# Optimization experiments

Hardware: AMD Instinct MI355X
Metric: run time of the kernel (lower is better)

## Reference

```python
import jax, jax.numpy as jnp
import numpy as np

K_H, K_W = 3, 3
STRIDE, PAD = 1, 1
GN_GROUPS = 32
EPS = 1e-5


def setup_inputs() -> dict:
    key = jax.random.key(0)
    k1, k2, k3 = jax.random.split(key, 3)
    B, C, H, W = 4, 256, 64, 64
    Cout = 256
    x = jax.random.normal(k1, (B, C, H, W), jnp.float32)
    offset = jax.random.normal(k2, (B, 2 * K_H * K_W, H, W), jnp.float32)
    weight = jax.random.normal(k3, (Cout, C, K_H, K_W), jnp.float32) * 0.02
    gamma = jnp.ones((Cout,), jnp.float32)
    beta = jnp.zeros((Cout,), jnp.float32)
    return {"x": x, "offset": offset, "weight": weight, "gamma": gamma, "beta": beta}


def _deform_conv(x, offset, weight):
    B, C, H, W = x.shape
    Cout = weight.shape[0]
    K = K_H * K_W
    Ho = (H + 2 * PAD - K_H) // STRIDE + 1
    Wo = (W + 2 * PAD - K_W) // STRIDE + 1
    ky, kx = jnp.meshgrid(jnp.arange(K_H), jnp.arange(K_W), indexing='ij')
    ky = ky.reshape(K).astype(x.dtype)
    kx = kx.reshape(K).astype(x.dtype)
    # base sampling positions per kernel tap
    py_base = (jnp.arange(Ho) * STRIDE - PAD).astype(x.dtype)[None, :] + ky[:, None]  # [K,Ho]
    px_base = (jnp.arange(Wo) * STRIDE - PAD).astype(x.dtype)[None, :] + kx[:, None]  # [K,Wo]
    off = offset.reshape(B, K, 2, Ho, Wo)  # mmcv layout: (dy, dx) pairs per tap
    py = py_base[None, :, :, None] + off[:, :, 0]  # [B,K,Ho,Wo]
    px = px_base[None, :, None, :] + off[:, :, 1]  # [B,K,Ho,Wo]
    y0 = jnp.floor(py)
    x0 = jnp.floor(px)
    ly = py - y0
    lx = px - x0
    xf = x.reshape(B, C, H * W)

    def gather(yi, xi):
        valid = (yi >= 0) & (yi <= H - 1) & (xi >= 0) & (xi <= W - 1)
        yc = jnp.clip(yi, 0, H - 1).astype(jnp.int32)
        xc = jnp.clip(xi, 0, W - 1).astype(jnp.int32)
        idx = yc * W + xc  # [B,K,Ho,Wo]
        vals = jax.vmap(lambda xb, ib: xb[:, ib])(xf, idx)  # [B,C,K,Ho,Wo]
        return vals * valid[:, None].astype(x.dtype)

    g00 = gather(y0, x0)
    g01 = gather(y0, x0 + 1)
    g10 = gather(y0 + 1, x0)
    g11 = gather(y0 + 1, x0 + 1)
    wy = ly[:, None]  # [B,1,K,Ho,Wo]
    wx = lx[:, None]
    val = ((1 - wy) * (1 - wx) * g00 + (1 - wy) * wx * g01
           + wy * (1 - wx) * g10 + wy * wx * g11)  # [B,C,K,Ho,Wo]
    return jnp.einsum('bckhw,ock->bohw', val, weight.reshape(Cout, C, K))


def reference(x, offset, weight, gamma, beta):
    y = _deform_conv(x, offset, weight)  # [B,Cout,Ho,Wo]
    B, C, H, W = y.shape
    yg = y.reshape(B, GN_GROUPS, C // GN_GROUPS, H, W)
    mean = jnp.mean(yg, axis=(2, 3, 4), keepdims=True)
    var = jnp.var(yg, axis=(2, 3, 4), keepdims=True)
    yn = ((yg - mean) * jax.lax.rsqrt(var + EPS)).reshape(B, C, H, W)
    out = yn * gamma[None, :, None, None] + beta[None, :, None, None]
    return jax.nn.relu(out)
```

## Files before the change

### kernel.cpp

```cpp
#include <hip/hip_runtime.h>

typedef unsigned short ushort_t;
typedef __bf16 bf16x8 __attribute__((ext_vector_type(8)));
typedef float f32x4 __attribute__((ext_vector_type(4)));
typedef void __attribute__((address_space(1))) gvoid_t;
typedef void __attribute__((address_space(3))) lvoid_t;

__device__ __forceinline__ float bflo(unsigned u) { return __builtin_bit_cast(float, u << 16); }
__device__ __forceinline__ float bfhi(unsigned u) { return __builtin_bit_cast(float, u & 0xffff0000u); }
__device__ __forceinline__ float bf2f(ushort_t v) {
  return __builtin_bit_cast(float, ((unsigned)v) << 16);
}
__device__ __forceinline__ unsigned f2bf_bits(float f) {
  unsigned u = __builtin_bit_cast(unsigned, f);
  return (u + 0x7fffu + ((u >> 16) & 1u)) >> 16;
}
__device__ __forceinline__ ushort_t f2bf(float f) { return (ushort_t)f2bf_bits(f); }

__global__ __launch_bounds__(256) void k_prep_w(const float* __restrict__ w,
                                                ushort_t* __restrict__ wb) {
  const int idx = blockIdx.x * 256 + threadIdx.x;
  const float* src = w + (size_t)idx * 9;
  #pragma unroll
  for (int k = 0; k < 9; ++k)
    wb[(k << 16) + idx] = f2bf(src[k]);
}

__global__ __launch_bounds__(256) void k_prep_x(const float* __restrict__ x,
                                                ushort_t* __restrict__ xt) {
  __shared__ ushort_t tile[64][68];
  const int bid = blockIdx.x;
  const int b = bid >> 8;
  const int ct = (bid >> 6) & 3;
  const int pt = bid & 63;
  const int t = threadIdx.x;
  const float* xb = x + ((size_t)(b * 256 + ct * 64)) * 4096 + pt * 64;
  #pragma unroll
  for (int i = 0; i < 16; ++i) {
    const int idx = t + 256 * i;
    const int c_l = idx >> 6, p_l = idx & 63;
    tile[c_l][p_l] = f2bf(xb[(size_t)c_l * 4096 + p_l]);
  }
  __syncthreads();
  ushort_t* xo = xt + ((size_t)(b * 4096 + pt * 64)) * 256 + ct * 64;
  #pragma unroll
  for (int i = 0; i < 16; ++i) {
    const int idx = t + 256 * i;
    const int p_l = idx >> 6, c_l = idx & 63;
    xo[(size_t)p_l * 256 + c_l] = tile[c_l][p_l];
  }
}

struct SMeta {
  float w00, w01, w10, w11;
  int i00, i01, i10, i11;
};
__device__ __forceinline__ SMeta meta_for(int h, int gw, int k, float oy, float ox) {
  SMeta m;
  const float py = (float)(h - 1 + k / 3) + oy;
  const float px = (float)(gw - 1 + k % 3) + ox;
  const float fy = floorf(py), fx = floorf(px);
  const float ly = py - fy, lx = px - fx;
  const int iy0 = (int)fy, ix0 = (int)fx;
  const float vy0 = (iy0 >= 0 && iy0 < 64) ? 1.f : 0.f;
  const float vy1 = (iy0 >= -1 && iy0 < 63) ? 1.f : 0.f;
  const float vx0 = (ix0 >= 0 && ix0 < 64) ? 1.f : 0.f;
  const float vx1 = (ix0 >= -1 && ix0 < 63) ? 1.f : 0.f;
  m.w00 = (1.f - ly) * (1.f - lx) * vy0 * vx0;
  m.w01 = (1.f - ly) * lx * vy0 * vx1;
  m.w10 = ly * (1.f - lx) * vy1 * vx0;
  m.w11 = ly * lx * vy1 * vx1;
  const int cy0 = min(max(iy0, 0), 63), cy1 = min(max(iy0 + 1, 0), 63);
  const int cx0 = min(max(ix0, 0), 63), cx1 = min(max(ix0 + 1, 0), 63);
  m.i00 = (cy0 * 64 + cx0) * 256;
  m.i01 = (cy0 * 64 + cx1) * 256;
  m.i10 = (cy1 * 64 + cx0) * 256;
  m.i11 = (cy1 * 64 + cx1) * 256;
  return m;
}

__device__ __forceinline__ unsigned lerp_pack(unsigned a, unsigned b, unsigned c, unsigned d,
                                              float w00, float w01, float w10, float w11) {
  float lo = w00 * bflo(a) + w01 * bflo(b) + w10 * bflo(c) + w11 * bflo(d);
  float hi = w00 * bfhi(a) + w01 * bfhi(b) + w10 * bfhi(c) + w11 * bfhi(d);
  return f2bf_bits(lo) | (f2bf_bits(hi) << 16);
}

template <int KH>
__device__ __forceinline__ void run_gemm(const float* __restrict__ offb,
                                         const ushort_t* __restrict__ xtb,
                                         const ushort_t* __restrict__ wb,
                                         ushort_t* Ab, ushort_t* Bb,
                                         int h, int s_w, int c8, int t,
                                         int wm, int wn, int wq, int wr,
                                         f32x4 (&acc)[2][4]) {
  float oy[5], ox[5];
  #pragma unroll
  for (int i = 0; i < 5; ++i) {
    oy[i] = offb[(2 * (KH * 4 + i)) * 4096];
    ox[i] = offb[(2 * (KH * 4 + i) + 1) * 4096];
  }

#define GATHER(N)                                                \
  {                                                              \
    const int c_ = KH * 18 + (N);                                \
    const int tap_ = c_ >> 2;                                    \
    const int loc_ = tap_ - KH * 4;                              \
    const int c0_ = (c_ & 3) << 6;                               \
    m = meta_for(h, s_w, tap_, oy[loc_], ox[loc_]);              \
    const int cc_ = c0_ + c8 * 8;                                \
    q00 = *(const uint4*)(xtb + m.i00 + cc_);                    \
    q01 = *(const uint4*)(xtb + m.i01 + cc_);                    \
    q10 = *(const uint4*)(xtb + m.i10 + cc_);                    \
    q11 = *(const uint4*)(xtb + m.i11 + cc_);                    \
  }

#define B_ISSUE(N, BUF)                                                                        \
  {                                                                                            \
    const int c_ = KH * 18 + (N);                                                              \
    const int tap_ = c_ >> 2;                                                                  \
    const int c0_ = (c_ & 3) << 6;                                                             \
    _Pragma("unroll") for (int i_ = 0; i_ < 4; ++i_) {                                         \
      const int idx_ = i_ * 512 + t;                                                           \
      const int row_ = idx_ >> 3, slot_ = idx_ & 7;                                            \
      const ushort_t* g_ = wb + (tap_ << 16) + row_ * 256 + c0_ + ((slot_ ^ (row_ & 7)) << 3); \
      __builtin_amdgcn_global_load_lds(                                                        \
          (gvoid_t*)g_, (lvoid_t*)((char*)Bb + (BUF) * 32768 + idx_ * 16), 16, 0, 0);          \
    }                                                                                          \
  }

#define A_WRITE(BUF)                                                         \
  {                                                                          \
    uint4 r;                                                                 \
    r.x = lerp_pack(q00.x, q01.x, q10.x, q11.x, m.w00, m.w01, m.w10, m.w11); \
    r.y = lerp_pack(q00.y, q01.y, q10.y, q11.y, m.w00, m.w01, m.w10, m.w11); \
    r.z = lerp_pack(q00.z, q01.z, q10.z, q11.z, m.w00, m.w01, m.w10, m.w11); \
    r.w = lerp_pack(q00.w, q01.w, q10.w, q11.w, m.w00, m.w01, m.w10, m.w11); \
    *(uint4*)&Ab[(BUF) * 4096 + s_w * 64 + ((c8 ^ (s_w & 7)) << 3)] = r;     \
  }

  {
    SMeta m;
    uint4 q00, q01, q10, q11;
    B_ISSUE(0, 0);
    GATHER(0);
    A_WRITE(0);
  }
  __syncthreads();

  #pragma unroll
  for (int n = 0; n < 18; ++n) {
    const int cur = n & 1;
    const int nb = cur ^ 1;
    SMeta m;
    uint4 q00, q01, q10, q11;
    if (n < 17) {
      B_ISSUE(n + 1, nb);
      GATHER(n + 1);
    }
    #pragma unroll
    for (int ks = 0; ks < 2; ++ks) {
      bf16x8 af[2], bfr[4];
      #pragma unroll
      for (int tm = 0; tm < 2; ++tm) {
        const int row = wm * 32 + tm * 16 + wr;
        const int slot = (ks * 4 + wq) ^ (row & 7);
        af[tm] = *(const bf16x8*)&Ab[cur * 4096 + row * 64 + slot * 8];
      }
      #pragma unroll
      for (int tn = 0; tn < 4; ++tn) {
        const int row = wn * 64 + tn * 16 + wr;
        const int slot = (ks * 4 + wq) ^ (row & 7);
        bfr[tn] = *(const bf16x8*)&Bb[cur * 16384 + row * 64 + slot * 8];
      }
      #pragma unroll
      for (int tm = 0; tm < 2; ++tm)
        #pragma unroll
        for (int tn = 0; tn < 4; ++tn)
          acc[tm][tn] =
              __builtin_amdgcn_mfma_f32_16x16x32_bf16(af[tm], bfr[tn], acc[tm][tn], 0, 0, 0);
    }
    if (n < 17) {
      A_WRITE(nb);
      __syncthreads();
    }
  }
#undef GATHER
#undef B_ISSUE
#undef A_WRITE
}

__global__ __launch_bounds__(512) void k_gemm(const float* __restrict__ off,
                                              const ushort_t* __restrict__ xt,
                                              const ushort_t* __restrict__ wb,
                                              ushort_t* __restrict__ y0,
                                              ushort_t* __restrict__ y1) {
  __shared__ __attribute__((aligned(16))) ushort_t Abuf[2][64 * 64];
  __shared__ __attribute__((aligned(16))) ushort_t Bbuf[2][256 * 64];

  const int bid = blockIdx.x;
  const int rowid = bid & 255;
  const int kh = bid >> 8;
  const int lb = ((rowid & 7) << 5) | (rowid >> 3);
  const int b = lb >> 6;
  const int h = lb & 63;
  const int t = threadIdx.x;
  const int wave = t >> 6;
  const int lane = t & 63;
  const int wq = lane >> 4;
  const int wr = lane & 15;
  const int wm = wave >> 2;
  const int wn = wave & 3;
  const int s_w = t >> 3;
  const int c8 = t & 7;

  const f32x4 zero = {0.f, 0.f, 0.f, 0.f};
  f32x4 acc[2][4];
  #pragma unroll
  for (int i = 0; i < 2; ++i)
    #pragma unroll
    for (int j = 0; j < 4; ++j) acc[i][j] = zero;

  const ushort_t* xtb = xt + (size_t)b * 4096 * 256;
  const float* offb = off + (size_t)b * 18 * 4096 + h * 64 + s_w;

  if (kh == 0)
    run_gemm<0>(offb, xtb, wb, &Abuf[0][0], &Bbuf[0][0], h, s_w, c8, t, wm, wn, wq, wr, acc);
  else
    run_gemm<1>(offb, xtb, wb, &Abuf[0][0], &Bbuf[0][0], h, s_w, c8, t, wm, wn, wq, wr, acc);

  ushort_t* yb = (kh ? y1 : y0) + ((size_t)(b * 4096 + h * 64)) * 256;
  #pragma unroll
  for (int tm = 0; tm < 2; ++tm) {
    #pragma unroll
    for (int tn = 0; tn < 4; ++tn) {
      const int o = wn * 64 + tn * 16 + wr;
      #pragma unroll
      for (int r2 = 0; r2 < 4; ++r2) {
        const int ww = wm * 32 + tm * 16 + wq * 4 + r2;
        yb[ww * 256 + o] = f2bf(acc[tm][tn][r2]);
      }
    }
  }
}

__global__ __launch_bounds__(256) void k_comb(const ushort_t* __restrict__ y0,
                                              const ushort_t* __restrict__ y1,
                                              ushort_t* __restrict__ yc,
                                              float* __restrict__ stats) {
  const int bid = blockIdx.x;
  const int lb = ((bid & 7) << 5) | (bid >> 3);
  const int b = lb >> 6;
  const int sc = lb & 63;
  const int t = threadIdx.x;
  const int og = t & 31;
  const int s0 = t >> 5;
  const size_t base = ((size_t)(b * 4096 + sc * 64)) * 256 + og * 8;
  float sum = 0.f, ss = 0.f;
  #pragma unroll
  for (int i = 0; i < 8; ++i) {
    const size_t o8 = base + (size_t)(s0 + i * 8) * 256;
    const uint4 a = *(const uint4*)(y0 + o8);
    const uint4 c = *(const uint4*)(y1 + o8);
    uint4 r;
    {
      float vl = bflo(a.x) + bflo(c.x), vh = bfhi(a.x) + bfhi(c.x);
      r.x = f2bf_bits(vl) | (f2bf_bits(vh) << 16);
      sum += vl + vh; ss += vl * vl + vh * vh;
    }
    {
      float vl = bflo(a.y) + bflo(c.y), vh = bfhi(a.y) + bfhi(c.y);
      r.y = f2bf_bits(vl) | (f2bf_bits(vh) << 16);
      sum += vl + vh; ss += vl * vl + vh * vh;
    }
    {
      float vl = bflo(a.z) + bflo(c.z), vh = bfhi(a.z) + bfhi(c.z);
      r.z = f2bf_bits(vl) | (f2bf_bits(vh) << 16);
      sum += vl + vh; ss += vl * vl + vh * vh;
    }
    {
      float vl = bflo(a.w) + bflo(c.w), vh = bfhi(a.w) + bfhi(c.w);
      r.w = f2bf_bits(vl) | (f2bf_bits(vh) << 16);
      sum += vl + vh; ss += vl * vl + vh * vh;
    }
    *(uint4*)(yc + o8) = r;
  }
  sum += __shfl_xor(sum, 32, 64);
  ss += __shfl_xor(ss, 32, 64);
  if ((t & 63) < 32) {
    atomicAdd(&stats[(b * 32 + og) * 2], sum);
    atomicAdd(&stats[(b * 32 + og) * 2 + 1], ss);
  }
}

__global__ __launch_bounds__(256) void k_apply(const ushort_t* __restrict__ yc,
                                               const float* __restrict__ stats,
                                               const float* __restrict__ gamma,
                                               const float* __restrict__ beta,
                                               float* __restrict__ out) {
  __shared__ float tile[64][65];
  __shared__ float sm[8], sr[8], sg[64], sb[64];
  const int bid = blockIdx.x;
  const int lb = ((bid & 7) << 7) | (bid >> 3);
  const int b = lb >> 8;
  const int st = (lb >> 2) & 63;
  const int ot = lb & 3;
  const int t = threadIdx.x;
  if (t < 8) {
    const int g = ot * 8 + t;
    const float s1 = stats[(b * 32 + g) * 2];
    const float s2 = stats[(b * 32 + g) * 2 + 1];
    const float mean = s1 * (1.f / 32768.f);
    const float var = s2 * (1.f / 32768.f) - mean * mean;
    sm[t] = mean;
    sr[t] = rsqrtf(var + 1e-5f);
  }
  if (t < 64) {
    sg[t] = gamma[ot * 64 + t];
    sb[t] = beta[ot * 64 + t];
  }
  const ushort_t* yb = yc + ((size_t)(b * 4096 + st * 64)) * 256 + ot * 64;
  #pragma unroll
  for (int i = 0; i < 16; ++i) {
    const int idx = t + 256 * i;
    const int s_l = idx >> 6, o_l = idx & 63;
    tile[s_l][o_l] = bf2f(yb[(size_t)s_l * 256 + o_l]);
  }
  __syncthreads();
  float* ob = out + ((size_t)(b * 256 + ot * 64)) * 4096 + st * 64;
  #pragma unroll
  for (int i = 0; i < 16; ++i) {
    const int idx = t + 256 * i;
    const int o_l = idx >> 6, s_l = idx & 63;
    const int g = o_l >> 3;
    float v = (tile[s_l][o_l] - sm[g]) * sr[g] * sg[o_l] + sb[o_l];
    v = v > 0.f ? v : 0.f;
    ob[(size_t)o_l * 4096 + s_l] = v;
  }
}

extern "C" void kernel_launch(void* const* d_in, const int* in_sizes, int n_in,
                              void* d_out, int out_size, void* d_ws, size_t ws_size,
                              hipStream_t stream) {
  const float* x = (const float*)d_in[0];
  const float* off = (const float*)d_in[1];
  const float* w = (const float*)d_in[2];
  const float* gamma = (const float*)d_in[3];
  const float* beta = (const float*)d_in[4];
  float* out = (float*)d_out;

  char* ws = (char*)d_ws;
  ushort_t* y0 = (ushort_t*)(ws);
  ushort_t* y1 = (ushort_t*)(ws + 8388608);
  ushort_t* xt = (ushort_t*)(ws + 16777216);
  ushort_t* yc = xt;
  ushort_t* wb = (ushort_t*)(ws + 25165824);
  float* stats = (float*)(ws + 26345472);

  hipMemsetAsync(stats, 0, 1024, stream);
  k_prep_w<<<256, 256, 0, stream>>>(w, wb);
  k_prep_x<<<1024, 256, 0, stream>>>(x, xt);
  k_gemm<<<512, 512, 0, stream>>>(off, xt, wb, y0, y1);
  k_comb<<<256, 256, 0, stream>>>(y0, y1, yc, stats);
  k_apply<<<1024, 256, 0, stream>>>(yc, stats, gamma, beta, out);
}
```

Baseline: 87.46 us.

## Merge prep kernels, move transpose into combine pass, vectorize apply, add MFMA priority

The separate weight and activation prep kernels and the stats memset become one launch, which removes two launches. The combine kernel now does the channel-to-NCHW transpose through shared memory while reducing group stats, and writes bf16 in NCHW layout. That lets the apply kernel become a simple vectorized elementwise pass with a precomputed per-channel scale and shift. The GEMM loop also raises wave priority around its MFMA block. The trade-off is more atomics in the combine step and a wider combine grid.

```diff
diff --git a/kernel.cpp b/kernel.cpp
--- a/kernel.cpp
+++ b/kernel.cpp
@@ -17,23 +17,26 @@
 }
 __device__ __forceinline__ ushort_t f2bf(float f) { return (ushort_t)f2bf_bits(f); }
 
-__global__ __launch_bounds__(256) void k_prep_w(const float* __restrict__ w,
-                                                ushort_t* __restrict__ wb) {
-  const int idx = blockIdx.x * 256 + threadIdx.x;
-  const float* src = w + (size_t)idx * 9;
-  #pragma unroll
-  for (int k = 0; k < 9; ++k)
-    wb[(k << 16) + idx] = f2bf(src[k]);
-}
-
-__global__ __launch_bounds__(256) void k_prep_x(const float* __restrict__ x,
-                                                ushort_t* __restrict__ xt) {
+__global__ __launch_bounds__(256) void k_prep(const float* __restrict__ x,
+                                              const float* __restrict__ w,
+                                              ushort_t* __restrict__ xt,
+                                              ushort_t* __restrict__ wb,
+                                              float* __restrict__ stats) {
+  const int gid = blockIdx.x;
+  const int t = threadIdx.x;
+  if (gid >= 1024) {
+    if (gid == 1024) stats[t] = 0.f;
+    const int idx = (gid - 1024) * 256 + t;
+    const float* src = w + (size_t)idx * 9;
+    #pragma unroll
+    for (int k = 0; k < 9; ++k)
+      wb[(k << 16) + idx] = f2bf(src[k]);
+    return;
+  }
   __shared__ ushort_t tile[64][68];
-  const int bid = blockIdx.x;
-  const int b = bid >> 8;
-  const int ct = (bid >> 6) & 3;
-  const int pt = bid & 63;
-  const int t = threadIdx.x;
+  const int b = gid >> 8;
+  const int ct = (gid >> 6) & 3;
+  const int pt = gid & 63;
   const float* xb = x + ((size_t)(b * 256 + ct * 64)) * 4096 + pt * 64;
   #pragma unroll
   for (int i = 0; i < 16; ++i) {
@@ -173,12 +176,14 @@
         const int slot = (ks * 4 + wq) ^ (row & 7);
         bfr[tn] = *(const bf16x8*)&Bb[cur * 16384 + row * 64 + slot * 8];
       }
+      __builtin_amdgcn_s_setprio(1);
       #pragma unroll
       for (int tm = 0; tm < 2; ++tm)
         #pragma unroll
         for (int tn = 0; tn < 4; ++tn)
           acc[tm][tn] =
               __builtin_amdgcn_mfma_f32_16x16x32_bf16(af[tm], bfr[tn], acc[tm][tn], 0, 0, 0);
+      __builtin_amdgcn_s_setprio(0);
     }
     if (n < 17) {
       A_WRITE(nb);
@@ -248,95 +253,98 @@
                                               const ushort_t* __restrict__ y1,
                                               ushort_t* __restrict__ yc,
                                               float* __restrict__ stats) {
-  const int bid = blockIdx.x;
-  const int lb = ((bid & 7) << 5) | (bid >> 3);
-  const int b = lb >> 6;
-  const int sc = lb & 63;
-  const int t = threadIdx.x;
-  const int og = t & 31;
-  const int s0 = t >> 5;
-  const size_t base = ((size_t)(b * 4096 + sc * 64)) * 256 + og * 8;
-  float sum = 0.f, ss = 0.f;
-  #pragma unroll
-  for (int i = 0; i < 8; ++i) {
-    const size_t o8 = base + (size_t)(s0 + i * 8) * 256;
-    const uint4 a = *(const uint4*)(y0 + o8);
-    const uint4 c = *(const uint4*)(y1 + o8);
-    uint4 r;
-    {
-      float vl = bflo(a.x) + bflo(c.x), vh = bfhi(a.x) + bfhi(c.x);
-      r.x = f2bf_bits(vl) | (f2bf_bits(vh) << 16);
-      sum += vl + vh; ss += vl * vl + vh * vh;
-    }
-    {
-      float vl = bflo(a.y) + bflo(c.y), vh = bfhi(a.y) + bfhi(c.y);
-      r.y = f2bf_bits(vl) | (f2bf_bits(vh) << 16);
-      sum += vl + vh; ss += vl * vl + vh * vh;
-    }
-    {
-      float vl = bflo(a.z) + bflo(c.z), vh = bfhi(a.z) + bfhi(c.z);
-      r.z = f2bf_bits(vl) | (f2bf_bits(vh) << 16);
-      sum += vl + vh; ss += vl * vl + vh * vh;
-    }
-    {
-      float vl = bflo(a.w) + bflo(c.w), vh = bfhi(a.w) + bfhi(c.w);
-      r.w = f2bf_bits(vl) | (f2bf_bits(vh) << 16);
-      sum += vl + vh; ss += vl * vl + vh * vh;
-    }
-    *(uint4*)(yc + o8) = r;
-  }
-  sum += __shfl_xor(sum, 32, 64);
-  ss += __shfl_xor(ss, 32, 64);
-  if ((t & 63) < 32) {
-    atomicAdd(&stats[(b * 32 + og) * 2], sum);
-    atomicAdd(&stats[(b * 32 + og) * 2 + 1], ss);
-  }
-}
-
-__global__ __launch_bounds__(256) void k_apply(const ushort_t* __restrict__ yc,
-                                               const float* __restrict__ stats,
-                                               const float* __restrict__ gamma,
-                                               const float* __restrict__ beta,
-                                               float* __restrict__ out) {
   __shared__ float tile[64][65];
-  __shared__ float sm[8], sr[8], sg[64], sb[64];
   const int bid = blockIdx.x;
   const int lb = ((bid & 7) << 7) | (bid >> 3);
   const int b = lb >> 8;
   const int st = (lb >> 2) & 63;
   const int ot = lb & 3;
   const int t = threadIdx.x;
-  if (t < 8) {
-    const int g = ot * 8 + t;
-    const float s1 = stats[(b * 32 + g) * 2];
-    const float s2 = stats[(b * 32 + g) * 2 + 1];
-    const float mean = s1 * (1.f / 32768.f);
-    const float var = s2 * (1.f / 32768.f) - mean * mean;
-    sm[t] = mean;
-    sr[t] = rsqrtf(var + 1e-5f);
-  }
-  if (t < 64) {
-    sg[t] = gamma[ot * 64 + t];
-    sb[t] = beta[ot * 64 + t];
-  }
-  const ushort_t* yb = yc + ((size_t)(b * 4096 + st * 64)) * 256 + ot * 64;
-  #pragma unroll
-  for (int i = 0; i < 16; ++i) {
-    const int idx = t + 256 * i;
-    const int s_l = idx >> 6, o_l = idx & 63;
-    tile[s_l][o_l] = bf2f(yb[(size_t)s_l * 256 + o_l]);
+  const size_t ybase = ((size_t)(b * 4096 + st * 64)) * 256 + ot * 64;
+  float sum = 0.f, ss = 0.f;
+  #pragma unroll
+  for (int i = 0; i < 2; ++i) {
+    const int u = t + 256 * i;
+    const int s_l = u >> 3;
+    const int o8 = u & 7;
+    const size_t adr = ybase + (size_t)s_l * 256 + o8 * 8;
+    const uint4 a = *(const uint4*)(y0 + adr);
+    const uint4 c = *(const uint4*)(y1 + adr);
+    float v[8];
+    v[0] = bflo(a.x) + bflo(c.x); v[1] = bfhi(a.x) + bfhi(c.x);
+    v[2] = bflo(a.y) + bflo(c.y); v[3] = bfhi(a.y) + bfhi(c.y);
+    v[4] = bflo(a.z) + bflo(c.z); v[5] = bfhi(a.z) + bfhi(c.z);
+    v[6] = bflo(a.w) + bflo(c.w); v[7] = bfhi(a.w) + bfhi(c.w);
+    #pragma unroll
+    for (int j = 0; j < 8; ++j) {
+      sum += v[j];
+      ss += v[j] * v[j];
+      tile[s_l][o8 * 8 + j] = v[j];
+    }
+  }
+  #pragma unroll
+  for (int d = 8; d < 64; d <<= 1) {
+    sum += __shfl_xor(sum, d, 64);
+    ss += __shfl_xor(ss, d, 64);
+  }
+  if ((t & 63) < 8) {
+    const int g = ot * 8 + (t & 7);
+    atomicAdd(&stats[(b * 32 + g) * 2], sum);
+    atomicAdd(&stats[(b * 32 + g) * 2 + 1], ss);
   }
   __syncthreads();
-  float* ob = out + ((size_t)(b * 256 + ot * 64)) * 4096 + st * 64;
-  #pragma unroll
-  for (int i = 0; i < 16; ++i) {
-    const int idx = t + 256 * i;
-    const int o_l = idx >> 6, s_l = idx & 63;
-    const int g = o_l >> 3;
-    float v = (tile[s_l][o_l] - sm[g]) * sr[g] * sg[o_l] + sb[o_l];
-    v = v > 0.f ? v : 0.f;
-    ob[(size_t)o_l * 4096 + s_l] = v;
-  }
+  #pragma unroll
+  for (int i = 0; i < 2; ++i) {
+    const int u = t + 256 * i;
+    const int o_l = u >> 3;
+    const int s8 = u & 7;
+    float v[8];
+    #pragma unroll
+    for (int j = 0; j < 8; ++j) v[j] = tile[s8 * 8 + j][o_l];
+    uint4 r;
+    r.x = f2bf_bits(v[0]) | (f2bf_bits(v[1]) << 16);
+    r.y = f2bf_bits(v[2]) | (f2bf_bits(v[3]) << 16);
+    r.z = f2bf_bits(v[4]) | (f2bf_bits(v[5]) << 16);
+    r.w = f2bf_bits(v[6]) | (f2bf_bits(v[7]) << 16);
+    *(uint4*)(yc + ((size_t)(b * 256 + ot * 64 + o_l)) * 4096 + st * 64 + s8 * 8) = r;
+  }
+}
+
+__global__ __launch_bounds__(256) void k_apply(const ushort_t* __restrict__ yc,
+                                               const float* __restrict__ stats,
+                                               const float* __restrict__ gamma,
+                                               const float* __restrict__ beta,
+                                               float* __restrict__ out) {
+  const int bid = blockIdx.x;
+  const int lb = ((bid & 7) << 8) | (bid >> 3);
+  const size_t base = (size_t)lb * 2048 + threadIdx.x * 8;
+  const int b = (int)(base >> 20);
+  const int o = (int)((base >> 12) & 255);
+  const int g = o >> 3;
+  const float s1 = stats[(b * 32 + g) * 2];
+  const float s2 = stats[(b * 32 + g) * 2 + 1];
+  const float mean = s1 * (1.f / 32768.f);
+  const float var = s2 * (1.f / 32768.f) - mean * mean;
+  const float rstd = rsqrtf(var + 1e-5f);
+  const float sc = rstd * gamma[o];
+  const float sh = beta[o] - mean * sc;
+  const uint4 a = *(const uint4*)(yc + base);
+  float v[8];
+  v[0] = bflo(a.x); v[1] = bfhi(a.x);
+  v[2] = bflo(a.y); v[3] = bfhi(a.y);
+  v[4] = bflo(a.z); v[5] = bfhi(a.z);
+  v[6] = bflo(a.w); v[7] = bfhi(a.w);
+  float4 f0, f1;
+  f0.x = fmaxf(v[0] * sc + sh, 0.f);
+  f0.y = fmaxf(v[1] * sc + sh, 0.f);
+  f0.z = fmaxf(v[2] * sc + sh, 0.f);
+  f0.w = fmaxf(v[3] * sc + sh, 0.f);
+  f1.x = fmaxf(v[4] * sc + sh, 0.f);
+  f1.y = fmaxf(v[5] * sc + sh, 0.f);
+  f1.z = fmaxf(v[6] * sc + sh, 0.f);
+  f1.w = fmaxf(v[7] * sc + sh, 0.f);
+  *(float4*)(out + base) = f0;
+  *(float4*)(out + base + 4) = f1;
 }
 
 extern "C" void kernel_launch(void* const* d_in, const int* in_sizes, int n_in,
@@ -357,10 +365,8 @@
   ushort_t* wb = (ushort_t*)(ws + 25165824);
   float* stats = (float*)(ws + 26345472);
 
-  hipMemsetAsync(stats, 0, 1024, stream);
-  k_prep_w<<<256, 256, 0, stream>>>(w, wb);
-  k_prep_x<<<1024, 256, 0, stream>>>(x, xt);
+  k_prep<<<1280, 256, 0, stream>>>(x, w, xt, wb, stats);
   k_gemm<<<512, 512, 0, stream>>>(off, xt, wb, y0, y1);
-  k_comb<<<256, 256, 0, stream>>>(y0, y1, yc, stats);
-  k_apply<<<1024, 256, 0, stream>>>(yc, stats, gamma, beta, out);
-}
+  k_comb<<<1024, 256, 0, stream>>>(y0, y1, yc, stats);
+  k_apply<<<2048, 256, 0, stream>>>(yc, stats, gamma, beta, out);
+}
```

Result: faster. 85.51 us (-2.2%).
